# Optimization experiments

Hardware: AMD Instinct MI355X
Metric: run time of the kernel (lower is better)

## Reference

```python
import jax, jax.numpy as jnp
import numpy as np

DIM = 768
NUM_HEADS = 12
HEAD_DIM = DIM // NUM_HEADS
SCALE = HEAD_DIM ** -0.5


def setup_inputs() -> dict:
    key = jax.random.key(0)
    ks = jax.random.split(key, 4)
    x = jax.random.normal(ks[0], (8, 1024, DIM), dtype=jnp.float32)
    # nn.Linear stores weight as [out, in]; we keep that convention.
    w_qkv = jax.random.normal(ks[1], (3 * DIM, DIM), dtype=jnp.float32) * (DIM ** -0.5)
    w_proj = jax.random.normal(ks[2], (DIM, DIM), dtype=jnp.float32) * (DIM ** -0.5)
    b_proj = jax.random.normal(ks[3], (DIM,), dtype=jnp.float32) * 0.02
    return {"x": x, "w_qkv": w_qkv, "w_proj": w_proj, "b_proj": b_proj}


def reference(x, w_qkv, w_proj, b_proj):
    B, N, C = x.shape
    H, D = NUM_HEADS, HEAD_DIM
    # qkv: [B, N, 3C] -> [3, B, H, N, D]
    qkv = jnp.einsum('bnc,oc->bno', x, w_qkv)
    qkv = qkv.reshape(B, N, 3, H, D).transpose(2, 0, 3, 1, 4)
    q, k, v = qkv[0] * SCALE, qkv[1], qkv[2]
    # attention scores [B, H, N, N]
    attn = jnp.einsum('bhnd,bhmd->bhnm', q, k)
    attn = jax.nn.softmax(attn, axis=-1)
    # weighted values -> [B, N, C]
    out = jnp.einsum('bhnm,bhmd->bhnd', attn, v)
    out = out.transpose(0, 2, 1, 3).reshape(B, N, C)
    # output projection
    return jnp.einsum('bnc,oc->bno', out, w_proj) + b_proj
```

## Files before the change

kernel.cpp:

```cpp
#include <hip/hip_runtime.h>
#include <hip/hip_bf16.h>
#include <math.h>


typedef unsigned short u16;
typedef __attribute__((ext_vector_type(8))) short bf16x8;
typedef __attribute__((ext_vector_type(4))) float f32x4;
typedef __attribute__((ext_vector_type(4))) unsigned int u32x4;

#define MFMA_BF16(a, b, c) __builtin_amdgcn_mfma_f32_16x16x32_bf16((a), (b), (c), 0, 0, 0)

static __device__ __forceinline__ void gld_lds16(const void* g, void* l) {
  __builtin_amdgcn_global_load_lds(
      (__attribute__((address_space(1))) void*)(g),
      (__attribute__((address_space(3))) void*)(l), 16, 0, 0);
}

static __device__ __forceinline__ u16 f2bf(float f) {
  __hip_bfloat16 h = __float2bfloat16(f);
  return *(u16*)&h;
}

static __device__ __forceinline__ float fast_exp2(float x) {
#if __has_builtin(__builtin_amdgcn_exp2f)
  return __builtin_amdgcn_exp2f(x);
#else
  return exp2f(x);
#endif
}

static __device__ __forceinline__ void conv4(const float* src, u16* dst, int i) {
  const float4 v = *(const float4*)(src + i);
  float f0 = v.x, f1 = v.y, f2 = v.z, f3 = v.w;
  if (!isfinite(f0)) f0 = 0.f;
  if (!isfinite(f1)) f1 = 0.f;
  if (!isfinite(f2)) f2 = 0.f;
  if (!isfinite(f3)) f3 = 0.f;
  ushort4 o;
  o.x = f2bf(f0); o.y = f2bf(f1); o.z = f2bf(f2); o.w = f2bf(f3);
  *(ushort4*)(dst + i) = o;
}

__global__ __launch_bounds__(256) void convert_kernel(
    const float* __restrict__ src, u16* __restrict__ dst, int n)
{
  const int i = (blockIdx.x * 256 + threadIdx.x) * 4;
  if (i < n) conv4(src, dst, i);
}

__global__ __launch_bounds__(256) void convert2_kernel(
    const float* __restrict__ a, u16* __restrict__ da, int na_blk,
    const float* __restrict__ b, u16* __restrict__ db)
{
  const int blk = blockIdx.x;
  if (blk < na_blk) {
    conv4(a, da, (blk * 256 + threadIdx.x) * 4);
  } else {
    conv4(b, db, ((blk - na_blk) * 256 + threadIdx.x) * 4);
  }
}

__device__ __forceinline__ void gemm_tile_768(
    const u16* __restrict__ A, const u16* __restrict__ B,
    int m0, int n0, u16* ldsA, u16* ldsB, f32x4 acc[4][4])
{
  const int tid  = threadIdx.x;
  const int lane = tid & 63;
  const int wave = tid >> 6;
  const int quad = lane >> 4;
  const int l16  = lane & 15;
  const int wm = wave >> 1, wn = wave & 1;

  const u16* gA[4]; const u16* gB[4]; int ldsoff[4];
#pragma unroll
  for (int it = 0; it < 4; ++it) {
    const int c   = it * 256 + tid;
    const int row = c >> 3;
    const int cc  = (c & 7) ^ (row & 7);
    gA[it] = A + (size_t)(m0 + row) * 768 + cc * 8;
    gB[it] = B + (size_t)(n0 + row) * 768 + cc * 8;
    ldsoff[it] = (it * 256 + wave * 64) * 8;
  }

  for (int kt = 0; kt < 12; ++kt) {
    __syncthreads();
#pragma unroll
    for (int it = 0; it < 4; ++it) {
      gld_lds16(gA[it] + kt * 64, ldsA + ldsoff[it]);
      gld_lds16(gB[it] + kt * 64, ldsB + ldsoff[it]);
    }
    __syncthreads();
#pragma unroll
    for (int kc = 0; kc < 2; ++kc) {
      bf16x8 av[4], bv[4];
#pragma unroll
      for (int i = 0; i < 4; ++i) {
        const int rowA = wm * 64 + i * 16 + l16;
        av[i] = *(const bf16x8*)(ldsA + rowA * 64 + (((kc * 4 + quad) ^ (rowA & 7)) * 8));
        const int rowB = wn * 64 + i * 16 + l16;
        bv[i] = *(const bf16x8*)(ldsB + rowB * 64 + (((kc * 4 + quad) ^ (rowB & 7)) * 8));
      }
#pragma unroll
      for (int i = 0; i < 4; ++i)
#pragma unroll
        for (int j = 0; j < 4; ++j)
          acc[i][j] = MFMA_BF16(av[i], bv[j], acc[i][j]);
    }
  }
}


__global__ __launch_bounds__(256, 2) void qkv_gemm_kernel(
    const u16* __restrict__ X, const u16* __restrict__ W,
    u16* __restrict__ Qb, u16* __restrict__ Kb, u16* __restrict__ Vt)
{
  __shared__ alignas(16) u16 lds[2 * 128 * 64];
  u16* ldsA = lds;
  u16* ldsB = lds + 128 * 64;
  const int n0 = blockIdx.x * 128;
  const int m0 = blockIdx.y * 128;
  f32x4 acc[4][4];
  const f32x4 zero = {0.f, 0.f, 0.f, 0.f};
#pragma unroll
  for (int i = 0; i < 4; ++i)
#pragma unroll
    for (int j = 0; j < 4; ++j) acc[i][j] = zero;

  gemm_tile_768(X, W, m0, n0, ldsA, ldsB, acc);

  const int tid = threadIdx.x, lane = tid & 63, wave = tid >> 6;
  const int quad = lane >> 4, l16 = lane & 15;
  const int wm = wave >> 1, wn = wave & 1;

  const int which = blockIdx.x / 6;
  const bool isV = (which == 2);
  const float sc = (which == 0) ? 0.180336880f : 1.0f;
  u16* ep = lds;

  __syncthreads();
#pragma unroll
  for (int i = 0; i < 4; ++i)
#pragma unroll
    for (int j = 0; j < 4; ++j)
#pragma unroll
      for (int r = 0; r < 4; ++r) {
        const int m_l = wm * 64 + i * 16 + quad * 4 + r;
        const int o_l = wn * 64 + j * 16 + l16;
        const int row = isV ? o_l : m_l;
        const int col = isV ? m_l : o_l;
        const int ch  = col >> 3;
        const int chs = (ch & 8) | ((ch & 7) ^ (row & 7));
        ep[row * 128 + chs * 8 + (col & 7)] = f2bf(acc[i][j][r] * sc);
      }
  __syncthreads();

  const int row  = tid >> 1, half = tid & 1;
  const int b_   = m0 >> 10;
  const int nb   = m0 & 1023;
  const int oc0  = n0 - which * 768;
  u16* dst;
  if (!isV) {
    const int h = (oc0 >> 6) + half;
    dst = (which == 0 ? Qb : Kb) + (((size_t)(b_ * 12 + h)) * 1024 + nb + row) * 64;
  } else {
    const int h = (oc0 >> 6) + (row >> 6);
    const int d = row & 63;
    dst = Vt + (((size_t)(b_ * 12 + h)) * 64 + d) * 1024 + nb + half * 64;
  }
#pragma unroll
  for (int c = 0; c < 8; ++c) {
    const int chs = half * 8 + (c ^ (row & 7));
    *(u32x4*)(dst + c * 8) = *(const u32x4*)(ep + row * 128 + chs * 8);
  }
}

__global__ __launch_bounds__(256, 2) void proj_gemm_kernel(
    const u16* __restrict__ A, const u16* __restrict__ W,
    const float* __restrict__ bias, float* __restrict__ out)
{
  __shared__ alignas(16) u16 ldsA[128 * 64];
  __shared__ alignas(16) u16 ldsB[128 * 64];
  const int n0 = blockIdx.x * 128;
  const int m0 = blockIdx.y * 128;
  f32x4 acc[4][4];
  const f32x4 zero = {0.f, 0.f, 0.f, 0.f};
#pragma unroll
  for (int i = 0; i < 4; ++i)
#pragma unroll
    for (int j = 0; j < 4; ++j) acc[i][j] = zero;

  gemm_tile_768(A, W, m0, n0, ldsA, ldsB, acc);

  const int tid = threadIdx.x, lane = tid & 63, wave = tid >> 6;
  const int quad = lane >> 4, l16 = lane & 15;
  const int wm = wave >> 1, wn = wave & 1;
#pragma unroll
  for (int j = 0; j < 4; ++j) {
    const int o = n0 + wn * 64 + j * 16 + l16;
    const float bv = bias[o];
#pragma unroll
    for (int i = 0; i < 4; ++i)
#pragma unroll
      for (int r = 0; r < 4; ++r) {
        const int m = m0 + wm * 64 + i * 16 + quad * 4 + r;
        out[(size_t)m * 768 + o] = acc[i][j][r] + bv;
      }
  }
}

__global__ __launch_bounds__(256, 3) void attn_kernel(
    const u16* __restrict__ Q, const u16* __restrict__ K,
    const u16* __restrict__ Vt, __hip_bfloat16* __restrict__ O)
{
  __shared__ alignas(16) u16 ldsK[64 * 64];
  __shared__ alignas(16) u16 ldsV[64 * 64];
  __shared__ alignas(16) u16 pbuf[4 * 32 * 72];
  const int bh = blockIdx.x;
  const int qb = blockIdx.y;
  const int tid = threadIdx.x;
  const int wave = tid >> 6, lane = tid & 63;
  const int quad = lane >> 4, l16 = lane & 15;
  u16* pw = pbuf + wave * (32 * 72);

  const int q0 = qb * 128 + wave * 32;
  const u16* Kbh = K  + (size_t)bh * (1024 * 64);
  const u16* Vbh = Vt + (size_t)bh * (64 * 1024);

  const int c0   = tid;
  const int row0 = c0 >> 3,          slot0 = c0 & 7;
  const int row1 = (c0 + 256) >> 3,  slot1 = c0 & 7;
  const int cc0 = slot0 ^ (row0 & 7), cc1 = slot1 ^ (row1 & 7);
  const u16* gK0 = Kbh + (size_t)row0 * 64 + cc0 * 8;
  const u16* gK1 = Kbh + (size_t)row1 * 64 + cc1 * 8;
  const u16* gV0 = Vbh + (size_t)row0 * 1024 + cc0 * 8;
  const u16* gV1 = Vbh + (size_t)row1 * 1024 + cc1 * 8;
  const int ldso0 = (wave * 64) * 8, ldso1 = (256 + wave * 64) * 8;

  bf16x8 aQ0[2], aQ1[2];
#pragma unroll
  for (int s = 0; s < 2; ++s) {
    const u16* qp = Q + ((size_t)bh * 1024 + q0 + s * 16 + l16) * 64 + quad * 8;
    aQ0[s] = *(const bf16x8*)qp;
    aQ1[s] = *(const bf16x8*)(qp + 32);
  }

  f32x4 oacc[2][4];
  const f32x4 zero = {0.f, 0.f, 0.f, 0.f};
#pragma unroll
  for (int s = 0; s < 2; ++s)
#pragma unroll
    for (int db = 0; db < 4; ++db) oacc[s][db] = zero;
  float lacc[2][4] = {{0.f, 0.f, 0.f, 0.f}, {0.f, 0.f, 0.f, 0.f}};

  for (int kt = 0; kt < 16; ++kt) {
    __syncthreads();
    gld_lds16(gK0 + (size_t)kt * 64 * 64, ldsK + ldso0);
    gld_lds16(gK1 + (size_t)kt * 64 * 64, ldsK + ldso1);
    gld_lds16(gV0 + kt * 64, ldsV + ldso0);
    gld_lds16(gV1 + kt * 64, ldsV + ldso1);
    __syncthreads();

    bf16x8 kb0[4], kb1[4];
#pragma unroll
    for (int t = 0; t < 4; ++t) {
      const int row = t * 16 + l16;
      kb0[t] = *(const bf16x8*)(ldsK + row * 64 + (((0 * 4 + quad) ^ (row & 7)) * 8));
      kb1[t] = *(const bf16x8*)(ldsK + row * 64 + (((1 * 4 + quad) ^ (row & 7)) * 8));
    }
#pragma unroll
    for (int s = 0; s < 2; ++s) {
#pragma unroll
      for (int t = 0; t < 4; ++t) {
        f32x4 z = zero;
        z = MFMA_BF16(aQ0[s], kb0[t], z);
        z = MFMA_BF16(aQ1[s], kb1[t], z);
#pragma unroll
        for (int r = 0; r < 4; ++r) {
          const float p = fast_exp2(z[r]);
          lacc[s][r] += p;
          pw[(s * 16 + quad * 4 + r) * 72 + t * 16 + l16] = f2bf(p);
        }
      }
    }
    asm volatile("" ::: "memory");
    bf16x8 pa0[2], pa1[2];
#pragma unroll
    for (int s = 0; s < 2; ++s) {
      const u16* pb = pw + (s * 16 + l16) * 72 + quad * 8;
      pa0[s] = *(const bf16x8*)pb;
      pa1[s] = *(const bf16x8*)(pb + 32);
    }
#pragma unroll
    for (int db = 0; db < 4; ++db) {
      const int row = db * 16 + l16;
      const bf16x8 v0 = *(const bf16x8*)(ldsV + row * 64 + (((0 * 4 + quad) ^ (row & 7)) * 8));
      const bf16x8 v1 = *(const bf16x8*)(ldsV + row * 64 + (((1 * 4 + quad) ^ (row & 7)) * 8));
#pragma unroll
      for (int s = 0; s < 2; ++s) {
        oacc[s][db] = MFMA_BF16(pa0[s], v0, oacc[s][db]);
        oacc[s][db] = MFMA_BF16(pa1[s], v1, oacc[s][db]);
      }
    }
  }

  const int b = bh / 12, h = bh - (bh / 12) * 12;
#pragma unroll
  for (int s = 0; s < 2; ++s) {
#pragma unroll
    for (int r = 0; r < 4; ++r) {
      float lsum = lacc[s][r];
      lsum += __shfl_xor(lsum, 1);
      lsum += __shfl_xor(lsum, 2);
      lsum += __shfl_xor(lsum, 4);
      lsum += __shfl_xor(lsum, 8);
      const float inv = 1.f / lsum;
      const int n = q0 + s * 16 + quad * 4 + r;
      __hip_bfloat16* orow = O + ((size_t)b * 1024 + n) * 768 + h * 64;
#pragma unroll
      for (int db = 0; db < 4; ++db)
        orow[db * 16 + l16] = __float2bfloat16(oacc[s][db][r] * inv);
    }
  }
}

extern "C" void kernel_launch(void* const* d_in, const int* in_sizes, int n_in,
                              void* d_out, int out_size, void* d_ws, size_t ws_size,
                              hipStream_t stream) {
  const float* x      = (const float*)d_in[0];
  const float* w_qkv  = (const float*)d_in[1];
  const float* w_proj = (const float*)d_in[2];
  const float* b_proj = (const float*)d_in[3];
  float* out = (float*)d_out;

  char* ws = (char*)d_ws;
  const size_t SEG = (size_t)96 * 1024 * 64 * sizeof(u16);
  u16* xb   = (u16*)(ws + 0 * SEG);
  u16* Qb   = (u16*)(ws + 1 * SEG);
  u16* Kb   = (u16*)(ws + 2 * SEG);
  u16* AO   = (u16*)(ws + 3 * SEG);
  u16* Vt   = (u16*)(ws + 4 * SEG);
  u16* wqb  = (u16*)(ws + 5 * SEG);
  u16* wpb  = (u16*)(ws + 5 * SEG + 3538944);

  const int nx = 8 * 1024 * 768, nq = 2304 * 768, np = 768 * 768;
  convert_kernel <<<nx / 1024, 256, 0, stream>>>(x, xb, nx);
  convert2_kernel<<<(nq + np) / 1024, 256, 0, stream>>>(w_qkv, wqb, nq / 1024,
                                                        w_proj, wpb);

  qkv_gemm_kernel<<<dim3(18, 64), 256, 0, stream>>>(xb, wqb, Qb, Kb, Vt);
  attn_kernel    <<<dim3(96, 8), 256, 0, stream>>>(Qb, Kb, Vt, (__hip_bfloat16*)AO);
  proj_gemm_kernel<<<dim3(6, 64), 256, 0, stream>>>(AO, wpb, b_proj, out);
}
```

Before: 194.4 us.

## Merge conversion kernels, shrink proj GEMM tile, double attention KV tile

The three fp32-to-bf16 conversions now run in one launch instead of two. The projection GEMM uses 128x64 tiles, so the grid grows from 384 to 768 blocks to fill the GPU better. Attention loads 128-key K/V tiles per iteration and processes them in two 64-key phases, halving the barrier and load rounds. The cost is more LDS per attention block, which may limit occupancy at 3 blocks per CU, and less reuse per tile in the projection GEMM.

```diff
diff --git a/kernel.cpp b/kernel.cpp
--- a/kernel.cpp
+++ b/kernel.cpp
@@ -41,23 +41,15 @@
   *(ushort4*)(dst + i) = o;
 }
 
-__global__ __launch_bounds__(256) void convert_kernel(
-    const float* __restrict__ src, u16* __restrict__ dst, int n)
-{
-  const int i = (blockIdx.x * 256 + threadIdx.x) * 4;
-  if (i < n) conv4(src, dst, i);
-}
-
-__global__ __launch_bounds__(256) void convert2_kernel(
-    const float* __restrict__ a, u16* __restrict__ da, int na_blk,
-    const float* __restrict__ b, u16* __restrict__ db)
+__global__ __launch_bounds__(256) void convert3_kernel(
+    const float* __restrict__ x,  u16* __restrict__ xb,
+    const float* __restrict__ wq, u16* __restrict__ wqb,
+    const float* __restrict__ wp, u16* __restrict__ wpb)
 {
   const int blk = blockIdx.x;
-  if (blk < na_blk) {
-    conv4(a, da, (blk * 256 + threadIdx.x) * 4);
-  } else {
-    conv4(b, db, ((blk - na_blk) * 256 + threadIdx.x) * 4);
-  }
+  if (blk < 6144)      conv4(x,  xb,  (blk * 256 + threadIdx.x) * 4);
+  else if (blk < 7872) conv4(wq, wqb, ((blk - 6144) * 256 + threadIdx.x) * 4);
+  else                 conv4(wp, wpb, ((blk - 7872) * 256 + threadIdx.x) * 4);
 }
 
 __device__ __forceinline__ void gemm_tile_768(
@@ -179,41 +171,81 @@
     const float* __restrict__ bias, float* __restrict__ out)
 {
   __shared__ alignas(16) u16 ldsA[128 * 64];
-  __shared__ alignas(16) u16 ldsB[128 * 64];
-  const int n0 = blockIdx.x * 128;
+  __shared__ alignas(16) u16 ldsB[64 * 64];
+  const int n0 = blockIdx.x * 64;
   const int m0 = blockIdx.y * 128;
-  f32x4 acc[4][4];
-  const f32x4 zero = {0.f, 0.f, 0.f, 0.f};
-#pragma unroll
-  for (int i = 0; i < 4; ++i)
-#pragma unroll
-    for (int j = 0; j < 4; ++j) acc[i][j] = zero;
-
-  gemm_tile_768(A, W, m0, n0, ldsA, ldsB, acc);
-
   const int tid = threadIdx.x, lane = tid & 63, wave = tid >> 6;
   const int quad = lane >> 4, l16 = lane & 15;
-  const int wm = wave >> 1, wn = wave & 1;
-#pragma unroll
-  for (int j = 0; j < 4; ++j) {
-    const int o = n0 + wn * 64 + j * 16 + l16;
-    const float bv = bias[o];
-#pragma unroll
-    for (int i = 0; i < 4; ++i)
+
+  const u16* gA[4]; const u16* gB[2]; int loA[4], loB[2];
+#pragma unroll
+  for (int it = 0; it < 4; ++it) {
+    const int c = it * 256 + tid, row = c >> 3, cc = (c & 7) ^ (row & 7);
+    gA[it] = A + (size_t)(m0 + row) * 768 + cc * 8;
+    loA[it] = (it * 256 + wave * 64) * 8;
+  }
+#pragma unroll
+  for (int it = 0; it < 2; ++it) {
+    const int c = it * 256 + tid, row = c >> 3, cc = (c & 7) ^ (row & 7);
+    gB[it] = W + (size_t)(n0 + row) * 768 + cc * 8;
+    loB[it] = (it * 256 + wave * 64) * 8;
+  }
+
+  f32x4 acc[2][4];
+  const f32x4 zero = {0.f, 0.f, 0.f, 0.f};
+#pragma unroll
+  for (int s = 0; s < 2; ++s)
+#pragma unroll
+    for (int t = 0; t < 4; ++t) acc[s][t] = zero;
+
+  for (int kt = 0; kt < 12; ++kt) {
+    __syncthreads();
+#pragma unroll
+    for (int it = 0; it < 4; ++it) gld_lds16(gA[it] + kt * 64, ldsA + loA[it]);
+#pragma unroll
+    for (int it = 0; it < 2; ++it) gld_lds16(gB[it] + kt * 64, ldsB + loB[it]);
+    __syncthreads();
+#pragma unroll
+    for (int kc = 0; kc < 2; ++kc) {
+      bf16x8 av[2], bv[4];
+#pragma unroll
+      for (int s = 0; s < 2; ++s) {
+        const int rowA = wave * 32 + s * 16 + l16;
+        av[s] = *(const bf16x8*)(ldsA + rowA * 64 + (((kc * 4 + quad) ^ (rowA & 7)) * 8));
+      }
+#pragma unroll
+      for (int t = 0; t < 4; ++t) {
+        const int rowB = t * 16 + l16;
+        bv[t] = *(const bf16x8*)(ldsB + rowB * 64 + (((kc * 4 + quad) ^ (rowB & 7)) * 8));
+      }
+#pragma unroll
+      for (int s = 0; s < 2; ++s)
+#pragma unroll
+        for (int t = 0; t < 4; ++t)
+          acc[s][t] = MFMA_BF16(av[s], bv[t], acc[s][t]);
+    }
+  }
+
+  float bv4[4];
+#pragma unroll
+  for (int t = 0; t < 4; ++t) bv4[t] = bias[n0 + t * 16 + l16];
+#pragma unroll
+  for (int s = 0; s < 2; ++s)
+#pragma unroll
+    for (int t = 0; t < 4; ++t)
 #pragma unroll
       for (int r = 0; r < 4; ++r) {
-        const int m = m0 + wm * 64 + i * 16 + quad * 4 + r;
-        out[(size_t)m * 768 + o] = acc[i][j][r] + bv;
-      }
-  }
+        const int m = m0 + wave * 32 + s * 16 + quad * 4 + r;
+        out[(size_t)m * 768 + n0 + t * 16 + l16] = acc[s][t][r] + bv4[t];
+      }
 }
 
 __global__ __launch_bounds__(256, 3) void attn_kernel(
     const u16* __restrict__ Q, const u16* __restrict__ K,
     const u16* __restrict__ Vt, __hip_bfloat16* __restrict__ O)
 {
-  __shared__ alignas(16) u16 ldsK[64 * 64];
-  __shared__ alignas(16) u16 ldsV[64 * 64];
+  __shared__ alignas(16) u16 ldsK[128 * 64];
+  __shared__ alignas(16) u16 ldsV[64 * 128];
   __shared__ alignas(16) u16 pbuf[4 * 32 * 72];
   const int bh = blockIdx.x;
   const int qb = blockIdx.y;
@@ -226,15 +258,22 @@
   const u16* Kbh = K  + (size_t)bh * (1024 * 64);
   const u16* Vbh = Vt + (size_t)bh * (64 * 1024);
 
-  const int c0   = tid;
-  const int row0 = c0 >> 3,          slot0 = c0 & 7;
-  const int row1 = (c0 + 256) >> 3,  slot1 = c0 & 7;
-  const int cc0 = slot0 ^ (row0 & 7), cc1 = slot1 ^ (row1 & 7);
-  const u16* gK0 = Kbh + (size_t)row0 * 64 + cc0 * 8;
-  const u16* gK1 = Kbh + (size_t)row1 * 64 + cc1 * 8;
-  const u16* gV0 = Vbh + (size_t)row0 * 1024 + cc0 * 8;
-  const u16* gV1 = Vbh + (size_t)row1 * 1024 + cc1 * 8;
-  const int ldso0 = (wave * 64) * 8, ldso1 = (256 + wave * 64) * 8;
+  const u16* gK[4]; const u16* gV[4]; int loK[4], loV[4];
+#pragma unroll
+  for (int it = 0; it < 4; ++it) {
+    const int c = it * 256 + tid;
+    {
+      const int row = c >> 3, cc = (c & 7) ^ (row & 7);
+      gK[it] = Kbh + (size_t)row * 64 + cc * 8;
+      loK[it] = (it * 256 + wave * 64) * 8;
+    }
+    {
+      const int row = c >> 4, slot = c & 15;
+      const int cc = (slot & 8) | ((slot & 7) ^ (row & 7));
+      gV[it] = Vbh + (size_t)row * 1024 + cc * 8;
+      loV[it] = (it * 256 + wave * 64) * 8;
+    }
+  }
 
   bf16x8 aQ0[2], aQ1[2];
 #pragma unroll
@@ -252,53 +291,58 @@
     for (int db = 0; db < 4; ++db) oacc[s][db] = zero;
   float lacc[2][4] = {{0.f, 0.f, 0.f, 0.f}, {0.f, 0.f, 0.f, 0.f}};
 
-  for (int kt = 0; kt < 16; ++kt) {
-    __syncthreads();
-    gld_lds16(gK0 + (size_t)kt * 64 * 64, ldsK + ldso0);
-    gld_lds16(gK1 + (size_t)kt * 64 * 64, ldsK + ldso1);
-    gld_lds16(gV0 + kt * 64, ldsV + ldso0);
-    gld_lds16(gV1 + kt * 64, ldsV + ldso1);
-    __syncthreads();
-
-    bf16x8 kb0[4], kb1[4];
-#pragma unroll
-    for (int t = 0; t < 4; ++t) {
-      const int row = t * 16 + l16;
-      kb0[t] = *(const bf16x8*)(ldsK + row * 64 + (((0 * 4 + quad) ^ (row & 7)) * 8));
-      kb1[t] = *(const bf16x8*)(ldsK + row * 64 + (((1 * 4 + quad) ^ (row & 7)) * 8));
-    }
-#pragma unroll
-    for (int s = 0; s < 2; ++s) {
+  for (int kt = 0; kt < 8; ++kt) {
+    __syncthreads();
+#pragma unroll
+    for (int it = 0; it < 4; ++it) {
+      gld_lds16(gK[it] + (size_t)kt * 128 * 64, ldsK + loK[it]);
+      gld_lds16(gV[it] + kt * 128, ldsV + loV[it]);
+    }
+    __syncthreads();
+
+#pragma unroll
+    for (int ph = 0; ph < 2; ++ph) {
+      bf16x8 kb0[4], kb1[4];
 #pragma unroll
       for (int t = 0; t < 4; ++t) {
-        f32x4 z = zero;
-        z = MFMA_BF16(aQ0[s], kb0[t], z);
-        z = MFMA_BF16(aQ1[s], kb1[t], z);
-#pragma unroll
-        for (int r = 0; r < 4; ++r) {
-          const float p = fast_exp2(z[r]);
-          lacc[s][r] += p;
-          pw[(s * 16 + quad * 4 + r) * 72 + t * 16 + l16] = f2bf(p);
+        const int row = ph * 64 + t * 16 + l16;
+        kb0[t] = *(const bf16x8*)(ldsK + row * 64 + (((0 * 4 + quad) ^ (row & 7)) * 8));
+        kb1[t] = *(const bf16x8*)(ldsK + row * 64 + (((1 * 4 + quad) ^ (row & 7)) * 8));
+      }
+      asm volatile("" ::: "memory");
+#pragma unroll
+      for (int s = 0; s < 2; ++s) {
+#pragma unroll
+        for (int t = 0; t < 4; ++t) {
+          f32x4 z = zero;
+          z = MFMA_BF16(aQ0[s], kb0[t], z);
+          z = MFMA_BF16(aQ1[s], kb1[t], z);
+#pragma unroll
+          for (int r = 0; r < 4; ++r) {
+            const float p = fast_exp2(z[r]);
+            lacc[s][r] += p;
+            pw[(s * 16 + quad * 4 + r) * 72 + t * 16 + l16] = f2bf(p);
+          }
         }
       }
-    }
-    asm volatile("" ::: "memory");
-    bf16x8 pa0[2], pa1[2];
-#pragma unroll
-    for (int s = 0; s < 2; ++s) {
-      const u16* pb = pw + (s * 16 + l16) * 72 + quad * 8;
-      pa0[s] = *(const bf16x8*)pb;
-      pa1[s] = *(const bf16x8*)(pb + 32);
-    }
-#pragma unroll
-    for (int db = 0; db < 4; ++db) {
-      const int row = db * 16 + l16;
-      const bf16x8 v0 = *(const bf16x8*)(ldsV + row * 64 + (((0 * 4 + quad) ^ (row & 7)) * 8));
-      const bf16x8 v1 = *(const bf16x8*)(ldsV + row * 64 + (((1 * 4 + quad) ^ (row & 7)) * 8));
+      asm volatile("" ::: "memory");
+      bf16x8 pa0[2], pa1[2];
 #pragma unroll
       for (int s = 0; s < 2; ++s) {
-        oacc[s][db] = MFMA_BF16(pa0[s], v0, oacc[s][db]);
-        oacc[s][db] = MFMA_BF16(pa1[s], v1, oacc[s][db]);
+        const u16* pb = pw + (s * 16 + l16) * 72 + quad * 8;
+        pa0[s] = *(const bf16x8*)pb;
+        pa1[s] = *(const bf16x8*)(pb + 32);
+      }
+#pragma unroll
+      for (int db = 0; db < 4; ++db) {
+        const int d = db * 16 + l16;
+        const bf16x8 v0 = *(const bf16x8*)(ldsV + d * 128 + (ph * 8 + ((0 * 4 + quad) ^ (d & 7))) * 8);
+        const bf16x8 v1 = *(const bf16x8*)(ldsV + d * 128 + (ph * 8 + ((1 * 4 + quad) ^ (d & 7))) * 8);
+#pragma unroll
+        for (int s = 0; s < 2; ++s) {
+          oacc[s][db] = MFMA_BF16(pa0[s], v0, oacc[s][db]);
+          oacc[s][db] = MFMA_BF16(pa1[s], v1, oacc[s][db]);
+        }
       }
     }
   }
@@ -342,12 +386,8 @@
   u16* wqb  = (u16*)(ws + 5 * SEG);
   u16* wpb  = (u16*)(ws + 5 * SEG + 3538944);
 
-  const int nx = 8 * 1024 * 768, nq = 2304 * 768, np = 768 * 768;
-  convert_kernel <<<nx / 1024, 256, 0, stream>>>(x, xb, nx);
-  convert2_kernel<<<(nq + np) / 1024, 256, 0, stream>>>(w_qkv, wqb, nq / 1024,
-                                                        w_proj, wpb);
-
+  convert3_kernel<<<8448, 256, 0, stream>>>(x, xb, w_qkv, wqb, w_proj, wpb);
   qkv_gemm_kernel<<<dim3(18, 64), 256, 0, stream>>>(xb, wqb, Qb, Kb, Vt);
   attn_kernel    <<<dim3(96, 8), 256, 0, stream>>>(Qb, Kb, Vt, (__hip_bfloat16*)AO);
-  proj_gemm_kernel<<<dim3(6, 64), 256, 0, stream>>>(AO, wpb, b_proj, out);
-}
+  proj_gemm_kernel<<<dim3(12, 64), 256, 0, stream>>>(AO, wpb, b_proj, out);
+}
```

Result: no change. 191.5 us (-1.5%).
